# Kernel optimization log

Measured on AMD Instinct MI355X. Metric: run time of the kernel, lower is better.

The kernel has to match this reference:

```python
import jax, jax.numpy as jnp
import numpy as np

T, B, I, H, O = 2048, 128, 32, 128, 1


def setup_inputs() -> dict:
    key = jax.random.key(0)
    ks = jax.random.split(key, 5)
    X = jax.random.normal(ks[0], (T, B, I), dtype=jnp.float32)
    W_in = jax.random.normal(ks[1], (H, I), dtype=jnp.float32) / np.sqrt(I)
    W_hh = jax.random.normal(ks[2], (H, H), dtype=jnp.float32) / np.sqrt(H)
    rnn_bias = jnp.zeros((H,), dtype=jnp.float32)
    alpha = jax.random.uniform(ks[3], (H,), dtype=jnp.float32)
    value_W = jax.random.normal(ks[4], (O, H), dtype=jnp.float32) / np.sqrt(H)
    value_bias = jnp.zeros((O,), dtype=jnp.float32)
    return {"X": X, "W_in": W_in, "W_hh": W_hh, "rnn_bias": rnn_bias,
            "alpha": alpha, "value_W": value_W, "value_bias": value_bias}


def reference(X, W_in, W_hh, rnn_bias, alpha, value_W, value_bias):
    # X: (T, B, I). Precompute input projections for all timesteps at once.
    xproj = jnp.einsum('tbi,hi->tbh', X, W_in)  # (T, B, H)

    def step(h_prev, xp_t):
        h_tilde = jnp.tanh(xp_t + h_prev @ W_hh.T + rnn_bias)
        h = (1.0 - alpha) * h_prev + alpha * h_tilde  # per-unit leaky blend
        return h, h

    h0 = jnp.zeros((X.shape[1], W_hh.shape[0]), dtype=X.dtype)
    last_hidden, Z = jax.lax.scan(step, h0, xproj)  # Z: (T, B, H)
    V = value_bias + jnp.einsum('tbh,oh->tbo', Z, value_W)  # (T, B, O)
    return V, last_hidden
```

## Files before the change

kernel.cpp:

```cpp
#include <hip/hip_runtime.h>

#define TT 2048
#define BB 128
#define II 32
#define HH 128
#define NW (TT / 8)

typedef float v2f __attribute__((ext_vector_type(2)));
typedef float v4f __attribute__((ext_vector_type(4)));
typedef unsigned int u32;
typedef __attribute__((address_space(3))) u32 lds_u32;
typedef const __attribute__((address_space(1))) u32 glb_u32;

__device__ __forceinline__ v2f pk_fma(v2f a, v2f b, v2f c) {
    v2f d;
    asm("v_pk_fma_f32 %0, %1, %2, %3" : "=v"(d) : "v"(a), "v"(b), "v"(c));
    return d;
}
template <int CTRL>
__device__ __forceinline__ float dpp_mov(float p) {
    return __int_as_float(__builtin_amdgcn_update_dpp(0, __float_as_int(p), CTRL, 0xF, 0xF, true));
}
template <int CTRL>
__device__ __forceinline__ float dpp_add(float p) { return p + dpp_mov<CTRL>(p); }
template <int CTRL>
__device__ __forceinline__ float pair_red(float x, float y, bool sel) {
    float keep = sel ? y : x;
    float give = sel ? x : y;
    return keep + dpp_mov<CTRL>(give);
}

__global__ __launch_bounds__(256)
void vrnn_kernel(const float* __restrict__ X, const float* __restrict__ W_in,
                 const float* __restrict__ W_hh, const float* __restrict__ rnn_bias,
                 const float* __restrict__ alpha, const float* __restrict__ value_W,
                 const float* __restrict__ value_bias, float* __restrict__ out)
{
    const int b    = blockIdx.x;
    const int tid  = threadIdx.x;
    const int wave = tid >> 6;
    const int lane = tid & 63;
    const int g    = lane >> 4;
    const int j    = lane & 15;
    const int base = 32 * wave + 8 * g;

    __shared__ __align__(16) float xw[2][8][II];
    __shared__ __align__(16) float hbuf[2][192];
    __shared__ __align__(16) float vres[TT];

    if (wave == 0) {
        const float* src = X + (size_t)(lane >> 3) * (BB * II) + b * II + (lane & 7) * 4;
        __builtin_amdgcn_global_load_lds((glb_u32*)src, (lds_u32*)(&xw[0][0][0]), 16, 0, 0);
    }

    const float SC = 2.8853900817779268f;

    v2f wh[8][4], wi8[8], binit[8];
#pragma unroll
    for (int r = 0; r < 8; ++r) {
        const float* wr = W_hh + (size_t)(base + r) * HH + 8 * j;
        v4f a0 = *(const v4f*)(wr);
        v4f a1 = *(const v4f*)(wr + 4);
        wh[r][0] = (v2f){a0.x * SC, a0.y * SC}; wh[r][1] = (v2f){a0.z * SC, a0.w * SC};
        wh[r][2] = (v2f){a1.x * SC, a1.y * SC}; wh[r][3] = (v2f){a1.z * SC, a1.w * SC};
        v2f wiv  = *(const v2f*)(W_in + (size_t)(base + r) * II + 2 * j);
        wi8[r]   = (v2f){wiv.x * SC, wiv.y * SC};
        binit[r] = (v2f){ (j == 0) ? rnn_bias[base + r] * SC : 0.0f, 0.0f };
    }
    v2f vwc[4];
#pragma unroll
    for (int i = 0; i < 4; ++i) vwc[i] = *(const v2f*)(value_W + 8 * j + 2 * i);
    const bool  b0 = (j & 1) != 0;
    const bool  b1 = (j & 2) != 0;
    const bool  selhi = ((j >> 2) & 1) != 0;
    const int   rown2 = base + (j & 3) + 4 * ((j >> 2) & 1);
    const float al_own = alpha[rown2];
    const float nal2   = -2.0f * al_own;
    const float oneml  = 1.0f - al_own;
    const float vb     = value_bias[0];
    const int   woff = 12 * (4 * wave + g) + (j & 3) + 4 * ((j >> 2) & 1);

    float hreg = 0.0f;
    float hsum = al_own;
    v2f   xc_next;
    v2f   pinit[8];

    if (tid < 192) hbuf[1][tid] = 0.0f;
    __syncthreads();

    float* outV = out;
    float* outH = out + (size_t)TT * BB;

#define STEP(S_)                                                               \
    {                                                                          \
        const int t   = 8 * w + (S_);                                          \
        const int par = (S_) & 1;                                              \
                                    \
        const float* hb = &hbuf[par ^ 1][12 * j];                              \
        const v4f h0v = *(const v4f*)(hb);                                     \
        const v4f h1v = *(const v4f*)(hb + 4);                                 \
        v2f pin[8];                                                            \
        if ((S_) == 0) {                                                       \
            const v2f xc0 = *(const v2f*)(&xw[w & 1][0][2 * j]);               \
            _Pragma("unroll")                                                  \
            for (int r = 0; r < 8; ++r) pin[r] = pk_fma(wi8[r], xc0, binit[r]);\
        } else {                                                               \
            _Pragma("unroll")                                                  \
            for (int r = 0; r < 8; ++r) pin[r] = pinit[r];                     \
        }                                                                      \
        v2f hp[4] = { (v2f){h0v.x, h0v.y}, (v2f){h0v.z, h0v.w},                \
                      (v2f){h1v.x, h1v.y}, (v2f){h1v.z, h1v.w} };              \
        float p[8];                                                            \
        _Pragma("unroll")                                                      \
        for (int r = 0; r < 8; ++r) {                                          \
            v2f a = pin[r];                                                    \
            a = pk_fma(wh[r][0], hp[0], a);                                    \
            a = pk_fma(wh[r][1], hp[1], a);                                    \
            a = pk_fma(wh[r][2], hp[2], a);                                    \
            a = pk_fma(wh[r][3], hp[3], a);                                    \
            p[r] = a.x + a.y;                                                  \
        }                                                                      \
        float q0 = pair_red<0xB1>(p[0], p[1], b0);                             \
        float q1 = pair_red<0xB1>(p[2], p[3], b0);                             \
        float q2 = pair_red<0xB1>(p[4], p[5], b0);                             \
        float q3 = pair_red<0xB1>(p[6], p[7], b0);                             \
        float r0 = pair_red<0x4E>(q0, q1, b1);                                 \
        float r1 = pair_red<0x4E>(q2, q3, b1);                                 \
        r0 = dpp_add<0x124>(r0);  r1 = dpp_add<0x124>(r1);                     \
        r0 = dpp_add<0x128>(r0);  r1 = dpp_add<0x128>(r1);                     \
        const float pre = selhi ? r1 : r0;                                     \
        const float e  = __builtin_amdgcn_exp2f(pre);                          \
        const float rc = __builtin_amdgcn_rcpf(e + 1.0f);                      \
        hreg = fmaf(nal2, rc, hsum);                                           \
        hbuf[par][woff] = hreg;                                                \
                                                          \
        hsum = fmaf(oneml, hreg, al_own);                                      \
        if (wave == ((S_) & 3) && ((w | (S_)) != 0)) {                         \
            v2f vt = vwc[0] * hp[0];                                           \
            vt = pk_fma(vwc[1], hp[1], vt);                                    \
            vt = pk_fma(vwc[2], hp[2], vt);                                    \
            vt = pk_fma(vwc[3], hp[3], vt);                                    \
            float vs = vt.x + vt.y;                                            \
            vs = dpp_add<0xB1>(vs);                                            \
            vs = dpp_add<0x4E>(vs);                                            \
            vs = dpp_add<0x124>(vs);                                           \
            vs = dpp_add<0x128>(vs);                                           \
            if (lane == 0) vres[t - 1] = vb + vs;                              \
        }                                                                      \
        if ((S_) < 7) {                                                        \
            xc_next = *(const v2f*)(&xw[w & 1][(S_) + 1][2 * j]);              \
            _Pragma("unroll")                                                  \
            for (int r = 0; r < 8; ++r)                                        \
                pinit[r] = pk_fma(wi8[r], xc_next, binit[r]);                  \
        }                                                                      \
        if (wave == 0 && (S_) == 7)                                            \
            asm volatile("s_waitcnt vmcnt(0)" ::: "memory");                   \
        asm volatile("s_waitcnt lgkmcnt(0)" ::: "memory");                     \
        __builtin_amdgcn_s_barrier();                                          \
    }

    for (int w = 0; w < NW; ++w) {
        if (wave == 0 && w + 1 < NW) {
            const float* src = X + (size_t)((w + 1) * 8 + (lane >> 3)) * (BB * II)
                                 + b * II + (lane & 7) * 4;
            __builtin_amdgcn_global_load_lds((glb_u32*)src,
                (lds_u32*)(&xw[(w + 1) & 1][0][0]), 16, 0, 0);
        }
        STEP(0) STEP(1) STEP(2) STEP(3) STEP(4) STEP(5) STEP(6) STEP(7)
    }
#undef STEP

    if (wave == 0) {
        const float* hb = &hbuf[1][12 * j];
        const v4f h0v = *(const v4f*)(hb);
        const v4f h1v = *(const v4f*)(hb + 4);
        v2f hp[4] = { (v2f){h0v.x, h0v.y}, (v2f){h0v.z, h0v.w},
                      (v2f){h1v.x, h1v.y}, (v2f){h1v.z, h1v.w} };
        v2f vt = vwc[0] * hp[0];
        vt = pk_fma(vwc[1], hp[1], vt);
        vt = pk_fma(vwc[2], hp[2], vt);
        vt = pk_fma(vwc[3], hp[3], vt);
        float vs = vt.x + vt.y;
        vs = dpp_add<0xB1>(vs);
        vs = dpp_add<0x4E>(vs);
        vs = dpp_add<0x124>(vs);
        vs = dpp_add<0x128>(vs);
        if (lane == 0) vres[TT - 1] = vb + vs;
    }
    if (j < 8)
        outH[(size_t)b * HH + base + j] = hreg;
    __syncthreads();
#pragma unroll
    for (int i = 0; i < TT / 256; ++i)
        outV[(size_t)(i * 256 + tid) * BB + b] = vres[i * 256 + tid];
}

extern "C" void kernel_launch(void* const* d_in, const int* in_sizes, int n_in,
                              void* d_out, int out_size, void* d_ws, size_t ws_size,
                              hipStream_t stream) {
    const float* X      = (const float*)d_in[0];
    const float* W_in   = (const float*)d_in[1];
    const float* W_hh   = (const float*)d_in[2];
    const float* rbias  = (const float*)d_in[3];
    const float* alpha  = (const float*)d_in[4];
    const float* vW     = (const float*)d_in[5];
    const float* vbias  = (const float*)d_in[6];
    float* out = (float*)d_out;

    vrnn_kernel<<<dim3(BB), dim3(256), 0, stream>>>(X, W_in, W_hh, rbias, alpha, vW, vbias, out);
}
```

Before: 770.2 us.

## Process two batch elements per block with interleaved recurrences

Each block now handles two batch columns, with duplicated LDS hidden-state buffers, input staging and value-head reductions. The two independent recurrences are interleaved in every step so their FMA, DPP and transcendental chains can overlap, and the grid is halved. This amortizes barriers and weight registers over two sequences, but raises per-step work and register pressure while leaving half as many blocks on a GPU that was already underfilled.

```diff
diff --git a/kernel.cpp b/kernel.cpp
--- a/kernel.cpp
+++ b/kernel.cpp
@@ -36,7 +36,8 @@
                  const float* __restrict__ alpha, const float* __restrict__ value_W,
                  const float* __restrict__ value_bias, float* __restrict__ out)
 {
-    const int b    = blockIdx.x;
+    const int b0   = 2 * blockIdx.x;
+    const int b1   = b0 + 1;
     const int tid  = threadIdx.x;
     const int wave = tid >> 6;
     const int lane = tid & 63;
@@ -44,13 +45,19 @@
     const int j    = lane & 15;
     const int base = 32 * wave + 8 * g;
 
-    __shared__ __align__(16) float xw[2][8][II];
-    __shared__ __align__(16) float hbuf[2][192];
-    __shared__ __align__(16) float vres[TT];
+    __shared__ __align__(16) float xw0[2][8][II];
+    __shared__ __align__(16) float xw1[2][8][II];
+    __shared__ __align__(16) float hbuf0[2][192];
+    __shared__ __align__(16) float hbuf1[2][192];
+    __shared__ __align__(16) float vres[2][TT];
 
     if (wave == 0) {
-        const float* src = X + (size_t)(lane >> 3) * (BB * II) + b * II + (lane & 7) * 4;
-        __builtin_amdgcn_global_load_lds((glb_u32*)src, (lds_u32*)(&xw[0][0][0]), 16, 0, 0);
+        const float* src = X + (size_t)(lane >> 3) * (BB * II) + b0 * II + (lane & 7) * 4;
+        __builtin_amdgcn_global_load_lds((glb_u32*)src, (lds_u32*)(&xw0[0][0][0]), 16, 0, 0);
+    }
+    if (wave == 1) {
+        const float* src = X + (size_t)(lane >> 3) * (BB * II) + b1 * II + (lane & 7) * 4;
+        __builtin_amdgcn_global_load_lds((glb_u32*)src, (lds_u32*)(&xw1[0][0][0]), 16, 0, 0);
     }
 
     const float SC = 2.8853900817779268f;
@@ -70,8 +77,8 @@
     v2f vwc[4];
 #pragma unroll
     for (int i = 0; i < 4; ++i) vwc[i] = *(const v2f*)(value_W + 8 * j + 2 * i);
-    const bool  b0 = (j & 1) != 0;
-    const bool  b1 = (j & 2) != 0;
+    const bool  b0s = (j & 1) != 0;
+    const bool  b1s = (j & 2) != 0;
     const bool  selhi = ((j >> 2) & 1) != 0;
     const int   rown2 = base + (j & 3) + 4 * ((j >> 2) & 1);
     const float al_own = alpha[rown2];
@@ -80,12 +87,11 @@
     const float vb     = value_bias[0];
     const int   woff = 12 * (4 * wave + g) + (j & 3) + 4 * ((j >> 2) & 1);
 
-    float hreg = 0.0f;
-    float hsum = al_own;
-    v2f   xc_next;
-    v2f   pinit[8];
-
-    if (tid < 192) hbuf[1][tid] = 0.0f;
+    float hreg0 = 0.0f, hsum0 = al_own;
+    float hreg1 = 0.0f, hsum1 = al_own;
+    v2f   pinit0[8], pinit1[8];
+
+    if (tid < 192) { hbuf0[1][tid] = 0.0f; hbuf1[1][tid] = 0.0f; }
     __syncthreads();
 
     float* outV = out;
@@ -95,83 +101,133 @@
     {                                                                          \
         const int t   = 8 * w + (S_);                                          \
         const int par = (S_) & 1;                                              \
-                                    \
-        const float* hb = &hbuf[par ^ 1][12 * j];                              \
-        const v4f h0v = *(const v4f*)(hb);                                     \
-        const v4f h1v = *(const v4f*)(hb + 4);                                 \
-        v2f pin[8];                                                            \
+                                        \
+        const float* hbA = &hbuf0[par ^ 1][12 * j];                            \
+        const v4f hA0 = *(const v4f*)(hbA);                                    \
+        const v4f hA1 = *(const v4f*)(hbA + 4);                                \
+        const float* hbB = &hbuf1[par ^ 1][12 * j];                            \
+        const v4f hB0 = *(const v4f*)(hbB);                                    \
+        const v4f hB1 = *(const v4f*)(hbB + 4);                                \
+        v2f pinA[8], pinB[8];                                                  \
         if ((S_) == 0) {                                                       \
-            const v2f xc0 = *(const v2f*)(&xw[w & 1][0][2 * j]);               \
+            const v2f xcA = *(const v2f*)(&xw0[w & 1][0][2 * j]);              \
+            const v2f xcB = *(const v2f*)(&xw1[w & 1][0][2 * j]);              \
             _Pragma("unroll")                                                  \
-            for (int r = 0; r < 8; ++r) pin[r] = pk_fma(wi8[r], xc0, binit[r]);\
+            for (int r = 0; r < 8; ++r) {                                      \
+                pinA[r] = pk_fma(wi8[r], xcA, binit[r]);                       \
+                pinB[r] = pk_fma(wi8[r], xcB, binit[r]);                       \
+            }                                                                  \
         } else {                                                               \
             _Pragma("unroll")                                                  \
-            for (int r = 0; r < 8; ++r) pin[r] = pinit[r];                     \
-        }                                                                      \
-        v2f hp[4] = { (v2f){h0v.x, h0v.y}, (v2f){h0v.z, h0v.w},                \
-                      (v2f){h1v.x, h1v.y}, (v2f){h1v.z, h1v.w} };              \
-        float p[8];                                                            \
+            for (int r = 0; r < 8; ++r) { pinA[r] = pinit0[r]; pinB[r] = pinit1[r]; } \
+        }                                                                      \
+        v2f hpA[4] = { (v2f){hA0.x, hA0.y}, (v2f){hA0.z, hA0.w},               \
+                       (v2f){hA1.x, hA1.y}, (v2f){hA1.z, hA1.w} };             \
+        v2f hpB[4] = { (v2f){hB0.x, hB0.y}, (v2f){hB0.z, hB0.w},               \
+                       (v2f){hB1.x, hB1.y}, (v2f){hB1.z, hB1.w} };             \
+        float pA[8], pB[8];                                                    \
         _Pragma("unroll")                                                      \
         for (int r = 0; r < 8; ++r) {                                          \
-            v2f a = pin[r];                                                    \
-            a = pk_fma(wh[r][0], hp[0], a);                                    \
-            a = pk_fma(wh[r][1], hp[1], a);                                    \
-            a = pk_fma(wh[r][2], hp[2], a);                                    \
-            a = pk_fma(wh[r][3], hp[3], a);                                    \
-            p[r] = a.x + a.y;                                                  \
-        }                                                                      \
-        float q0 = pair_red<0xB1>(p[0], p[1], b0);                             \
-        float q1 = pair_red<0xB1>(p[2], p[3], b0);                             \
-        float q2 = pair_red<0xB1>(p[4], p[5], b0);                             \
-        float q3 = pair_red<0xB1>(p[6], p[7], b0);                             \
-        float r0 = pair_red<0x4E>(q0, q1, b1);                                 \
-        float r1 = pair_red<0x4E>(q2, q3, b1);                                 \
-        r0 = dpp_add<0x124>(r0);  r1 = dpp_add<0x124>(r1);                     \
-        r0 = dpp_add<0x128>(r0);  r1 = dpp_add<0x128>(r1);                     \
-        const float pre = selhi ? r1 : r0;                                     \
-        const float e  = __builtin_amdgcn_exp2f(pre);                          \
-        const float rc = __builtin_amdgcn_rcpf(e + 1.0f);                      \
-        hreg = fmaf(nal2, rc, hsum);                                           \
-        hbuf[par][woff] = hreg;                                                \
+            v2f a = pinA[r];                                                   \
+            a = pk_fma(wh[r][0], hpA[0], a);                                   \
+            a = pk_fma(wh[r][1], hpA[1], a);                                   \
+            a = pk_fma(wh[r][2], hpA[2], a);                                   \
+            a = pk_fma(wh[r][3], hpA[3], a);                                   \
+            pA[r] = a.x + a.y;                                                 \
+            v2f c = pinB[r];                                                   \
+            c = pk_fma(wh[r][0], hpB[0], c);                                   \
+            c = pk_fma(wh[r][1], hpB[1], c);                                   \
+            c = pk_fma(wh[r][2], hpB[2], c);                                   \
+            c = pk_fma(wh[r][3], hpB[3], c);                                   \
+            pB[r] = c.x + c.y;                                                 \
+        }                                                                      \
+        float qA0 = pair_red<0xB1>(pA[0], pA[1], b0s);                         \
+        float qA1 = pair_red<0xB1>(pA[2], pA[3], b0s);                         \
+        float qA2 = pair_red<0xB1>(pA[4], pA[5], b0s);                         \
+        float qA3 = pair_red<0xB1>(pA[6], pA[7], b0s);                         \
+        float qB0 = pair_red<0xB1>(pB[0], pB[1], b0s);                         \
+        float qB1 = pair_red<0xB1>(pB[2], pB[3], b0s);                         \
+        float qB2 = pair_red<0xB1>(pB[4], pB[5], b0s);                         \
+        float qB3 = pair_red<0xB1>(pB[6], pB[7], b0s);                         \
+        float rA0 = pair_red<0x4E>(qA0, qA1, b1s);                             \
+        float rA1 = pair_red<0x4E>(qA2, qA3, b1s);                             \
+        float rB0 = pair_red<0x4E>(qB0, qB1, b1s);                             \
+        float rB1 = pair_red<0x4E>(qB2, qB3, b1s);                             \
+        rA0 = dpp_add<0x124>(rA0); rA1 = dpp_add<0x124>(rA1);                  \
+        rB0 = dpp_add<0x124>(rB0); rB1 = dpp_add<0x124>(rB1);                  \
+        rA0 = dpp_add<0x128>(rA0); rA1 = dpp_add<0x128>(rA1);                  \
+        rB0 = dpp_add<0x128>(rB0); rB1 = dpp_add<0x128>(rB1);                  \
+        const float preA = selhi ? rA1 : rA0;                                  \
+        const float preB = selhi ? rB1 : rB0;                                  \
+        const float eA  = __builtin_amdgcn_exp2f(preA);                        \
+        const float eB  = __builtin_amdgcn_exp2f(preB);                        \
+        const float rcA = __builtin_amdgcn_rcpf(eA + 1.0f);                    \
+        const float rcB = __builtin_amdgcn_rcpf(eB + 1.0f);                    \
+        hreg0 = fmaf(nal2, rcA, hsum0);                                        \
+        hreg1 = fmaf(nal2, rcB, hsum1);                                        \
+        hbuf0[par][woff] = hreg0;                                              \
+        hbuf1[par][woff] = hreg1;                                              \
                                                           \
-        hsum = fmaf(oneml, hreg, al_own);                                      \
-        if (wave == ((S_) & 3) && ((w | (S_)) != 0)) {                         \
-            v2f vt = vwc[0] * hp[0];                                           \
-            vt = pk_fma(vwc[1], hp[1], vt);                                    \
-            vt = pk_fma(vwc[2], hp[2], vt);                                    \
-            vt = pk_fma(vwc[3], hp[3], vt);                                    \
-            float vs = vt.x + vt.y;                                            \
-            vs = dpp_add<0xB1>(vs);                                            \
-            vs = dpp_add<0x4E>(vs);                                            \
-            vs = dpp_add<0x124>(vs);                                           \
-            vs = dpp_add<0x128>(vs);                                           \
-            if (lane == 0) vres[t - 1] = vb + vs;                              \
+        hsum0 = fmaf(oneml, hreg0, al_own);                                    \
+        hsum1 = fmaf(oneml, hreg1, al_own);                                    \
+        if (((w | (S_)) != 0)) {                                               \
+            if (wave == ((S_) & 3)) {                                          \
+                v2f vt = vwc[0] * hpA[0];                                      \
+                vt = pk_fma(vwc[1], hpA[1], vt);                               \
+                vt = pk_fma(vwc[2], hpA[2], vt);                               \
+                vt = pk_fma(vwc[3], hpA[3], vt);                               \
+                float vs = vt.x + vt.y;                                        \
+                vs = dpp_add<0xB1>(vs); vs = dpp_add<0x4E>(vs);                \
+                vs = dpp_add<0x124>(vs); vs = dpp_add<0x128>(vs);              \
+                if (lane == 0) vres[0][t - 1] = vb + vs;                       \
+            }                                                                  \
+            if (wave == (((S_) + 2) & 3)) {                                    \
+                v2f vt = vwc[0] * hpB[0];                                      \
+                vt = pk_fma(vwc[1], hpB[1], vt);                               \
+                vt = pk_fma(vwc[2], hpB[2], vt);                               \
+                vt = pk_fma(vwc[3], hpB[3], vt);                               \
+                float vs = vt.x + vt.y;                                        \
+                vs = dpp_add<0xB1>(vs); vs = dpp_add<0x4E>(vs);                \
+                vs = dpp_add<0x124>(vs); vs = dpp_add<0x128>(vs);              \
+                if (lane == 0) vres[1][t - 1] = vb + vs;                       \
+            }                                                                  \
         }                                                                      \
         if ((S_) < 7) {                                                        \
-            xc_next = *(const v2f*)(&xw[w & 1][(S_) + 1][2 * j]);              \
+            const v2f xnA = *(const v2f*)(&xw0[w & 1][(S_) + 1][2 * j]);       \
+            const v2f xnB = *(const v2f*)(&xw1[w & 1][(S_) + 1][2 * j]);       \
             _Pragma("unroll")                                                  \
-            for (int r = 0; r < 8; ++r)                                        \
-                pinit[r] = pk_fma(wi8[r], xc_next, binit[r]);                  \
-        }                                                                      \
-        if (wave == 0 && (S_) == 7)                                            \
+            for (int r = 0; r < 8; ++r) {                                      \
+                pinit0[r] = pk_fma(wi8[r], xnA, binit[r]);                     \
+                pinit1[r] = pk_fma(wi8[r], xnB, binit[r]);                     \
+            }                                                                  \
+        }                                                                      \
+        if (wave <= 1 && (S_) == 7)                                            \
             asm volatile("s_waitcnt vmcnt(0)" ::: "memory");                   \
         asm volatile("s_waitcnt lgkmcnt(0)" ::: "memory");                     \
         __builtin_amdgcn_s_barrier();                                          \
     }
 
     for (int w = 0; w < NW; ++w) {
-        if (wave == 0 && w + 1 < NW) {
-            const float* src = X + (size_t)((w + 1) * 8 + (lane >> 3)) * (BB * II)
-                                 + b * II + (lane & 7) * 4;
-            __builtin_amdgcn_global_load_lds((glb_u32*)src,
-                (lds_u32*)(&xw[(w + 1) & 1][0][0]), 16, 0, 0);
+        if (w + 1 < NW) {
+            if (wave == 0) {
+                const float* src = X + (size_t)((w + 1) * 8 + (lane >> 3)) * (BB * II)
+                                     + b0 * II + (lane & 7) * 4;
+                __builtin_amdgcn_global_load_lds((glb_u32*)src,
+                    (lds_u32*)(&xw0[(w + 1) & 1][0][0]), 16, 0, 0);
+            }
+            if (wave == 1) {
+                const float* src = X + (size_t)((w + 1) * 8 + (lane >> 3)) * (BB * II)
+                                     + b1 * II + (lane & 7) * 4;
+                __builtin_amdgcn_global_load_lds((glb_u32*)src,
+                    (lds_u32*)(&xw1[(w + 1) & 1][0][0]), 16, 0, 0);
+            }
         }
         STEP(0) STEP(1) STEP(2) STEP(3) STEP(4) STEP(5) STEP(6) STEP(7)
     }
 #undef STEP
 
-    if (wave == 0) {
-        const float* hb = &hbuf[1][12 * j];
+    if (wave == 0 || wave == 1) {
+        const float* hb = (wave == 0) ? &hbuf0[1][12 * j] : &hbuf1[1][12 * j];
         const v4f h0v = *(const v4f*)(hb);
         const v4f h1v = *(const v4f*)(hb + 4);
         v2f hp[4] = { (v2f){h0v.x, h0v.y}, (v2f){h0v.z, h0v.w},
@@ -181,18 +237,20 @@
         vt = pk_fma(vwc[2], hp[2], vt);
         vt = pk_fma(vwc[3], hp[3], vt);
         float vs = vt.x + vt.y;
-        vs = dpp_add<0xB1>(vs);
-        vs = dpp_add<0x4E>(vs);
-        vs = dpp_add<0x124>(vs);
-        vs = dpp_add<0x128>(vs);
-        if (lane == 0) vres[TT - 1] = vb + vs;
-    }
-    if (j < 8)
-        outH[(size_t)b * HH + base + j] = hreg;
+        vs = dpp_add<0xB1>(vs); vs = dpp_add<0x4E>(vs);
+        vs = dpp_add<0x124>(vs); vs = dpp_add<0x128>(vs);
+        if (lane == 0) vres[wave][TT - 1] = vb + vs;
+    }
+    if (j < 8) {
+        outH[(size_t)b0 * HH + base + j] = hreg0;
+        outH[(size_t)b1 * HH + base + j] = hreg1;
+    }
     __syncthreads();
 #pragma unroll
-    for (int i = 0; i < TT / 256; ++i)
-        outV[(size_t)(i * 256 + tid) * BB + b] = vres[i * 256 + tid];
+    for (int i = 0; i < TT / 256; ++i) {
+        outV[(size_t)(i * 256 + tid) * BB + b0] = vres[0][i * 256 + tid];
+        outV[(size_t)(i * 256 + tid) * BB + b1] = vres[1][i * 256 + tid];
+    }
 }
 
 extern "C" void kernel_launch(void* const* d_in, const int* in_sizes, int n_in,
@@ -207,5 +265,5 @@
     const float* vbias  = (const float*)d_in[6];
     float* out = (float*)d_out;
 
-    vrnn_kernel<<<dim3(BB), dim3(256), 0, stream>>>(X, W_in, W_hh, rbias, alpha, vW, vbias, out);
-}
+    vrnn_kernel<<<dim3(BB / 2), dim3(256), 0, stream>>>(X, W_in, W_hh, rbias, alpha, vW, vbias, out);
+}
```

After: 1.272 ms. 65.2% more time.
